# Kernel tuning notes

Measured on AMD Instinct MI355X. Metric: run time of the kernel, lower is better.

The kernel has to match this reference:

```python
import jax, jax.numpy as jnp
import numpy as np

N_NODES = 1_000_000
N_GRAPHS = 8192
DIM = 64
FEAT = 64


def setup_inputs() -> dict:
    key = jax.random.key(0)
    ks = jax.random.split(key, 12)
    s = 0.05
    inp = {}
    inp["x"] = jax.random.normal(ks[0], (N_NODES, FEAT), jnp.float32)
    inp["batch"] = jnp.sort(jax.random.randint(ks[1], (N_NODES,), 0, N_GRAPHS, dtype=jnp.int32))
    inp["lin0_w"] = jax.random.normal(ks[2], (DIM, FEAT), jnp.float32) * s
    inp["lin0_b"] = jnp.zeros((DIM,), jnp.float32)
    inp["lin1_w"] = jax.random.normal(ks[3], (DIM, DIM), jnp.float32) * s
    inp["lin1_b"] = jnp.zeros((DIM,), jnp.float32)
    inp["gru_wih"] = jax.random.normal(ks[4], (3 * DIM, DIM), jnp.float32) * s
    inp["gru_whh"] = jax.random.normal(ks[5], (3 * DIM, DIM), jnp.float32) * s
    inp["gru_bih"] = jnp.zeros((3 * DIM,), jnp.float32)
    inp["gru_bhh"] = jnp.zeros((3 * DIM,), jnp.float32)
    inp["lstm_wih"] = jax.random.normal(ks[6], (4 * DIM, 2 * DIM), jnp.float32) * s
    inp["lstm_whh"] = jax.random.normal(ks[7], (4 * DIM, DIM), jnp.float32) * s
    inp["lstm_bih"] = jnp.zeros((4 * DIM,), jnp.float32)
    inp["lstm_bhh"] = jnp.zeros((4 * DIM,), jnp.float32)
    inp["lin2_w"] = jax.random.normal(ks[8], (DIM, 2 * DIM), jnp.float32) * s
    inp["lin2_b"] = jnp.zeros((DIM,), jnp.float32)
    inp["lin3_w"] = jax.random.normal(ks[9], (1, DIM), jnp.float32) * s
    inp["lin3_b"] = jnp.zeros((1,), jnp.float32)
    inp["n_graphs"] = N_GRAPHS
    return inp


def _gru_step(m, h, wih, whh, bih, bhh):
    # single-step PyTorch GRU semantics
    gi = m @ wih.T + bih          # [N, 3D]
    gh = h @ whh.T + bhh          # [N, 3D]
    ir, iz, in_ = jnp.split(gi, 3, axis=-1)
    hr, hz, hn = jnp.split(gh, 3, axis=-1)
    r = jax.nn.sigmoid(ir + hr)
    z = jax.nn.sigmoid(iz + hz)
    n = jnp.tanh(in_ + r * hn)
    return (1.0 - z) * n + z * h


def _segment_softmax(e, batch, n_graphs):
    m = jax.ops.segment_max(e, batch, num_segments=n_graphs)
    ex = jnp.exp(e - m[batch])
    s = jax.ops.segment_sum(ex, batch, num_segments=n_graphs)
    return ex / (s[batch] + 1e-16)


def reference(x, batch, lin0_w, lin0_b, lin1_w, lin1_b,
              gru_wih, gru_whh, gru_bih, gru_bhh,
              lstm_wih, lstm_whh, lstm_bih, lstm_bhh,
              lin2_w, lin2_b, lin3_w, lin3_b, n_graphs):
    dim = lin0_w.shape[0]
    out = jax.nn.relu(x @ lin0_w.T + lin0_b)   # [N, D]
    h = out
    for _ in range(3):
        m = jax.nn.relu(out @ lin1_w.T + lin1_b)
        h = _gru_step(m, h, gru_wih, gru_whh, gru_bih, gru_bhh)
        out = h

    # Set2Set, processing_steps = 3
    q_star = jnp.zeros((n_graphs, 2 * dim), out.dtype)
    hl = jnp.zeros((n_graphs, dim), out.dtype)
    cl = jnp.zeros((n_graphs, dim), out.dtype)
    for _ in range(3):
        gates = q_star @ lstm_wih.T + lstm_bih + hl @ lstm_whh.T + lstm_bhh  # [B, 4D]
        gi, gf, gg, go = jnp.split(gates, 4, axis=-1)
        cl = jax.nn.sigmoid(gf) * cl + jax.nn.sigmoid(gi) * jnp.tanh(gg)
        hl = jax.nn.sigmoid(go) * jnp.tanh(cl)
        q = hl                                   # [B, D]
        e = jnp.sum(out * q[batch], axis=-1)     # [N]
        a = _segment_softmax(e, batch, n_graphs) # [N]
        r = jax.ops.segment_sum(a[:, None] * out, batch, num_segments=n_graphs)  # [B, D]
        q_star = jnp.concatenate([q, r], axis=-1)

    y = jax.nn.relu(q_star @ lin2_w.T + lin2_b)
    y = y @ lin3_w.T + lin3_b
    return y.reshape(-1)
```

## Files before the change

kernel.cpp:

```cpp
#include <hip/hip_runtime.h>
#include <hip/hip_bf16.h>
#include <math.h>

#define TILES 6
#define MBLK 96

typedef __attribute__((ext_vector_type(8))) short bf8;
typedef __attribute__((ext_vector_type(4))) float f32x4;

#define MFMA(a, b, c) __builtin_amdgcn_mfma_f32_16x16x32_bf16(a, b, c, 0, 0, 0)

__device__ __forceinline__ float fast_rcp(float x) { return __builtin_amdgcn_rcpf(x); }
__device__ __forceinline__ float sigm(float x) { return fast_rcp(1.0f + __expf(-x)); }
__device__ __forceinline__ float tanh2(float x) { return fmaf(2.0f, fast_rcp(1.0f + __expf(-2.0f * x)), -1.0f); }

__device__ __forceinline__ unsigned short f2bf(float v) {
    union { __hip_bfloat16 b; unsigned short u; } cv;
    cv.b = __float2bfloat16(v);
    return cv.u;
}
__device__ __forceinline__ float bf2f(unsigned short u) {
    union { unsigned short u; __hip_bfloat16 b; } cv;
    cv.u = u;
    return __bfloat162float(cv.b);
}
__device__ __forceinline__ void split_tr(float v, unsigned short& hi, unsigned short& lo) {
    unsigned int uv = __builtin_bit_cast(unsigned int, v);
    hi = (unsigned short)(uv >> 16);
    float rem = v - __builtin_bit_cast(float, uv & 0xffff0000u);
    lo = f2bf(rem);
}
__device__ __forceinline__ f32x4 ntload4(const float* p) {
    return __builtin_nontemporal_load((const f32x4*)p);
}

__global__ void prep_kernel(const float* __restrict__ l0w, const float* __restrict__ l1w,
                            const float* __restrict__ gwih, const float* __restrict__ gwhh,
                            const float* __restrict__ lwih, const float* __restrict__ lwhh,
                            const float* __restrict__ l2w,
                            const int* __restrict__ batch,
                            unsigned short* __restrict__ whi, unsigned short* __restrict__ wlo,
                            float* __restrict__ liT, float* __restrict__ lhT,
                            float* __restrict__ l2T,
                            float* __restrict__ u, float* __restrict__ cl,
                            int* __restrict__ startp,
                            int n_nodes, int n_graphs)
{
    int tid = blockIdx.x * 256 + threadIdx.x;
    int nthreads = gridDim.x * 256;
    if (tid < 32768) {
        int e = tid & 7, lane = (tid >> 3) & 63, ks = (tid >> 9) & 1, jt = tid >> 10;
        const float* W; int jl;
        if (jt < 4)       { W = l0w;  jl = jt; }
        else if (jt < 8)  { W = l1w;  jl = jt - 4; }
        else if (jt < 20) { W = gwih; jl = jt - 8; }
        else              { W = gwhh; jl = jt - 20; }
        int j = jl * 16 + (lane & 15);
        int k = ks * 32 + (lane >> 4) * 8 + e;
        float v = W[j * 64 + k];
        unsigned short hi = f2bf(v);
        whi[tid] = hi;
        wlo[tid] = f2bf(v - bf2f(hi));
    }
    if (tid < 32768) liT[tid] = lwih[(tid & 255) * 128 + (tid >> 8)];
    if (tid < 16384) lhT[tid] = lwhh[(tid & 255) * 64 + (tid >> 8)];
    if (tid < 8192)  l2T[tid] = l2w[(tid & 63) * 128 + (tid >> 6)];
    if (tid <= n_graphs) {
        int lo = 0, hi = n_nodes;
        while (lo < hi) {
            int mid = (lo + hi) >> 1;
            if (batch[mid] < tid) lo = mid + 1; else hi = mid;
        }
        startp[tid] = lo;
    }
    for (int i = tid; i < n_graphs * 192; i += nthreads) u[i] = 0.0f;
    for (int i = tid; i < n_graphs * 64;  i += nthreads) cl[i] = 0.0f;
}

__launch_bounds__(256, 2)
__global__ void node_kernel(const float* __restrict__ x,
                            const unsigned short* __restrict__ whi,
                            const unsigned short* __restrict__ wlo,
                            const float* __restrict__ l0b, const float* __restrict__ l1b,
                            const float* __restrict__ gbih, const float* __restrict__ gbhh,
                            float* __restrict__ outv, int n_nodes)
{
    __shared__ unsigned short MHI[TILES * 1024], MLO[TILES * 1024];
    __shared__ unsigned short HHI[TILES * 1024], HLO[TILES * 1024];
    const int tid = threadIdx.x;
    const int w = tid >> 6, lane = tid & 63, c = lane & 15, g = lane >> 4;
    const long node0 = (long)blockIdx.x * MBLK;
    const int j = w * 16 + c;

    const float bR  = gbih[j] + gbhh[j];
    const float bZ  = gbih[64 + j] + gbhh[64 + j];
    const float bNI = gbih[128 + j];
    const float bNH = gbhh[128 + j];
    const float bL1 = l1b[j];
    const float bL0 = l0b[j];

    const int kgj = (j >> 3) & 3;
    const int koff2 = ((j >> 5) * 512) + (kgj * 128) + (j & 7);
    const int lane_swz = (lane & 48) | (c ^ g);

    const bf8* WH = (const bf8*)whi;
    const bf8* WL = (const bf8*)wlo;
#define LF(name, jt) \
    bf8 name##h0 = WH[((jt) * 2 + 0) * 64 + lane], name##h1 = WH[((jt) * 2 + 1) * 64 + lane], \
        name##l0 = WL[((jt) * 2 + 0) * 64 + lane], name##l1 = WL[((jt) * 2 + 1) * 64 + lane];
    LF(w0, w)
    LF(w1, 4 + w)
    LF(gir, 8 + w)  LF(giz, 12 + w)  LF(gin, 16 + w)
    LF(ghr, 20 + w) LF(ghz, 24 + w) LF(ghn, 28 + w)
#undef LF

    float hc[TILES][4];

#pragma unroll
    for (int t = 0; t < TILES; ++t) {
        long nd = node0 + t * 16 + c;
        if (nd >= n_nodes) nd = n_nodes - 1;
        const float* xp = x + nd * 64 + g * 8;
        float va[8], vb[8];
        {
            float4 u0 = *(const float4*)xp;
            float4 u1 = *(const float4*)(xp + 4);
            float4 u2 = *(const float4*)(xp + 32);
            float4 u3 = *(const float4*)(xp + 36);
            va[0] = u0.x; va[1] = u0.y; va[2] = u0.z; va[3] = u0.w;
            va[4] = u1.x; va[5] = u1.y; va[6] = u1.z; va[7] = u1.w;
            vb[0] = u2.x; vb[1] = u2.y; vb[2] = u2.z; vb[3] = u2.w;
            vb[4] = u3.x; vb[5] = u3.y; vb[6] = u3.z; vb[7] = u3.w;
        }
        bf8 xh0, xl0, xh1, xl1;
#pragma unroll
        for (int e = 0; e < 8; ++e) {
            unsigned short h0, l0, h1, l1;
            split_tr(va[e], h0, l0);
            split_tr(vb[e], h1, l1);
            xh0[e] = (short)h0; xl0[e] = (short)l0;
            xh1[e] = (short)h1; xl1[e] = (short)l1;
        }
        f32x4 acc = {bL0, bL0, bL0, bL0};
        acc = MFMA(xh0, w0h0, acc); acc = MFMA(xl0, w0h0, acc); acc = MFMA(xh0, w0l0, acc);
        acc = MFMA(xh1, w0h1, acc); acc = MFMA(xl1, w0h1, acc); acc = MFMA(xh1, w0l1, acc);
#pragma unroll
        for (int p = 0; p < 4; ++p) {
            float hv = fmaxf(acc[p], 0.0f);
            hc[t][p] = hv;
            int r = g * 4 + p;
            unsigned short hi, lo;
            split_tr(hv, hi, lo);
            int idx = t * 1024 + koff2 + ((r ^ kgj) << 3);
            HHI[idx] = hi;
            HLO[idx] = lo;
        }
    }
    __syncthreads();

    for (int iter = 0; iter < 3; ++iter) {
#pragma unroll
        for (int t = 0; t < TILES; ++t) {
            const bf8* hh = (const bf8*)&HHI[t * 1024];
            const bf8* hl = (const bf8*)&HLO[t * 1024];
            bf8 ah0 = hh[lane_swz], ah1 = hh[64 + lane_swz];
            bf8 al0 = hl[lane_swz], al1 = hl[64 + lane_swz];
            f32x4 acc = {bL1, bL1, bL1, bL1};
            acc = MFMA(ah0, w1h0, acc); acc = MFMA(al0, w1h0, acc); acc = MFMA(ah0, w1l0, acc);
            acc = MFMA(ah1, w1h1, acc); acc = MFMA(al1, w1h1, acc); acc = MFMA(ah1, w1l1, acc);
#pragma unroll
            for (int p = 0; p < 4; ++p) {
                float mv = fmaxf(acc[p], 0.0f);
                int r = g * 4 + p;
                unsigned short hi, lo;
                split_tr(mv, hi, lo);
                int idx = t * 1024 + koff2 + ((r ^ kgj) << 3);
                MHI[idx] = hi;
                MLO[idx] = lo;
            }
        }
        __syncthreads();

#pragma unroll
        for (int t = 0; t < TILES; ++t) {
            const bf8* mh = (const bf8*)&MHI[t * 1024];
            const bf8* ml = (const bf8*)&MLO[t * 1024];
            const bf8* hh = (const bf8*)&HHI[t * 1024];
            const bf8* hl = (const bf8*)&HLO[t * 1024];
            bf8 amh0 = mh[lane_swz], amh1 = mh[64 + lane_swz];
            bf8 aml0 = ml[lane_swz], aml1 = ml[64 + lane_swz];
            bf8 ahh0 = hh[lane_swz], ahh1 = hh[64 + lane_swz];
            bf8 ahl0 = hl[lane_swz], ahl1 = hl[64 + lane_swz];

            f32x4 aR  = {bR, bR, bR, bR};
            f32x4 aZ  = {bZ, bZ, bZ, bZ};
            f32x4 aNI = {bNI, bNI, bNI, bNI};
            f32x4 aNH = {bNH, bNH, bNH, bNH};

            aR = MFMA(amh0, girh0, aR); aR = MFMA(aml0, girh0, aR); aR = MFMA(amh0, girl0, aR);
            aR = MFMA(amh1, girh1, aR); aR = MFMA(aml1, girh1, aR); aR = MFMA(amh1, girl1, aR);
            aR = MFMA(ahh0, ghrh0, aR); aR = MFMA(ahl0, ghrh0, aR); aR = MFMA(ahh0, ghrl0, aR);
            aR = MFMA(ahh1, ghrh1, aR); aR = MFMA(ahl1, ghrh1, aR); aR = MFMA(ahh1, ghrl1, aR);

            aZ = MFMA(amh0, gizh0, aZ); aZ = MFMA(aml0, gizh0, aZ); aZ = MFMA(amh0, gizl0, aZ);
            aZ = MFMA(amh1, gizh1, aZ); aZ = MFMA(aml1, gizh1, aZ); aZ = MFMA(amh1, gizl1, aZ);
            aZ = MFMA(ahh0, ghzh0, aZ); aZ = MFMA(ahl0, ghzh0, aZ); aZ = MFMA(ahh0, ghzl0, aZ);
            aZ = MFMA(ahh1, ghzh1, aZ); aZ = MFMA(ahl1, ghzh1, aZ); aZ = MFMA(ahh1, ghzl1, aZ);

            aNI = MFMA(amh0, ginh0, aNI); aNI = MFMA(aml0, ginh0, aNI); aNI = MFMA(amh0, ginl0, aNI);
            aNI = MFMA(amh1, ginh1, aNI); aNI = MFMA(aml1, ginh1, aNI); aNI = MFMA(amh1, ginl1, aNI);

            aNH = MFMA(ahh0, ghnh0, aNH); aNH = MFMA(ahl0, ghnh0, aNH); aNH = MFMA(ahh0, ghnl0, aNH);
            aNH = MFMA(ahh1, ghnh1, aNH); aNH = MFMA(ahl1, ghnh1, aNH); aNH = MFMA(ahh1, ghnl1, aNH);

#pragma unroll
            for (int p = 0; p < 4; ++p) {
                float rg = sigm(aR[p]);
                float zg = sigm(aZ[p]);
                float ng = tanh2(aNI[p] + rg * aNH[p]);
                hc[t][p] = (1.0f - zg) * ng + zg * hc[t][p];
            }
        }

        if (iter < 2) {
            __syncthreads();
#pragma unroll
            for (int t = 0; t < TILES; ++t)
#pragma unroll
                for (int p = 0; p < 4; ++p) {
                    int r = g * 4 + p;
                    unsigned short hi, lo;
                    split_tr(hc[t][p], hi, lo);
                    int idx = t * 1024 + koff2 + ((r ^ kgj) << 3);
                    HHI[idx] = hi;
                    HLO[idx] = lo;
                }
            __syncthreads();
        }
    }

#pragma unroll
    for (int t = 0; t < TILES; ++t)
#pragma unroll
        for (int p = 0; p < 4; ++p) {
            long nd = node0 + t * 16 + g * 4 + p;
            if (nd < n_nodes) outv[nd * 64 + j] = hc[t][p];
        }
}

__global__ void lstm_kernel(const float* __restrict__ liT, const float* __restrict__ lhT,
                            const float* __restrict__ lbih, const float* __restrict__ lbhh,
                            float* __restrict__ u, float* __restrict__ cl, int n_graphs)
{
    const int t = threadIdx.x;
    const int g = blockIdx.x * 4 + (t >> 6);
    const int d = t & 63;
    if (g >= n_graphs) return;
    float* ug = u + (size_t)g * 192;

    float aI = lbih[d]       + lbhh[d];
    float aF = lbih[64 + d]  + lbhh[64 + d];
    float aG = lbih[128 + d] + lbhh[128 + d];
    float aO = lbih[192 + d] + lbhh[192 + d];
    for (int k = 0; k < 128; ++k) {
        float uv = ug[k];
        const float* wr = liT + k * 256;
        aI = fmaf(wr[d], uv, aI);
        aF = fmaf(wr[64 + d], uv, aF);
        aG = fmaf(wr[128 + d], uv, aG);
        aO = fmaf(wr[192 + d], uv, aO);
    }
    for (int k = 0; k < 64; ++k) {
        float hv = ug[128 + k];
        const float* wr = lhT + k * 256;
        aI = fmaf(wr[d], hv, aI);
        aF = fmaf(wr[64 + d], hv, aF);
        aG = fmaf(wr[128 + d], hv, aG);
        aO = fmaf(wr[192 + d], hv, aO);
    }
    float c = sigm(aF) * cl[(size_t)g * 64 + d] + sigm(aI) * tanh2(aG);
    cl[(size_t)g * 64 + d] = c;
    float h = sigm(aO) * tanh2(c);
    ug[d] = h;
    ug[128 + d] = h;
}

__global__ void attn_kernel(const float* __restrict__ outv,
                            const int* __restrict__ startp,
                            float* __restrict__ u, int n_graphs)
{
    __shared__ float qS[64];
    __shared__ float mG[16], sG[16];
    __shared__ float rG[16][64];

    const int g = blockIdx.x;
    const int t = threadIdx.x;
    const int s0 = startp[g];
    const int cnt = startp[g + 1] - s0;
    if (t < 64) qS[t] = u[(size_t)g * 192 + t];
    __syncthreads();

    const int grp = t >> 4, l = t & 15;
    const float q0 = qS[l * 4], q1 = qS[l * 4 + 1], q2 = qS[l * 4 + 2], q3 = qS[l * 4 + 3];

    float m = -INFINITY, s = 0.0f;
    float r0 = 0.0f, r1 = 0.0f, r2 = 0.0f, r3 = 0.0f;

    int n = grp;
    for (; n + 16 < cnt; n += 32) {
        f32x4 va = ntload4(outv + (size_t)(s0 + n) * 64 + l * 4);
        f32x4 vb = ntload4(outv + (size_t)(s0 + n + 16) * 64 + l * 4);
        float ea = fmaf(va.x, q0, fmaf(va.y, q1, fmaf(va.z, q2, va.w * q3)));
        float eb = fmaf(vb.x, q0, fmaf(vb.y, q1, fmaf(vb.z, q2, vb.w * q3)));
#pragma unroll
        for (int o = 1; o < 16; o <<= 1) {
            ea += __shfl_xor(ea, o);
            eb += __shfl_xor(eb, o);
        }
        float mn = fmaxf(m, fmaxf(ea, eb));
        float sc = __expf(m - mn);
        float wa = __expf(ea - mn);
        float wb = __expf(eb - mn);
        s = s * sc + wa + wb;
        r0 = fmaf(r0, sc, fmaf(wa, va.x, wb * vb.x));
        r1 = fmaf(r1, sc, fmaf(wa, va.y, wb * vb.y));
        r2 = fmaf(r2, sc, fmaf(wa, va.z, wb * vb.z));
        r3 = fmaf(r3, sc, fmaf(wa, va.w, wb * vb.w));
        m = mn;
    }
    if (n < cnt) {
        f32x4 va = ntload4(outv + (size_t)(s0 + n) * 64 + l * 4);
        float ea = fmaf(va.x, q0, fmaf(va.y, q1, fmaf(va.z, q2, va.w * q3)));
#pragma unroll
        for (int o = 1; o < 16; o <<= 1) ea += __shfl_xor(ea, o);
        float mn = fmaxf(m, ea);
        float sc = __expf(m - mn);
        float wa = __expf(ea - mn);
        s = s * sc + wa;
        r0 = fmaf(r0, sc, wa * va.x);
        r1 = fmaf(r1, sc, wa * va.y);
        r2 = fmaf(r2, sc, wa * va.z);
        r3 = fmaf(r3, sc, wa * va.w);
        m = mn;
    }

    if (l == 0) { mG[grp] = m; sG[grp] = s; }
    rG[grp][l * 4 + 0] = r0;
    rG[grp][l * 4 + 1] = r1;
    rG[grp][l * 4 + 2] = r2;
    rG[grp][l * 4 + 3] = r3;
    __syncthreads();

    if (t < 64) {
        float M = -INFINITY;
#pragma unroll
        for (int j2 = 0; j2 < 16; ++j2) M = fmaxf(M, mG[j2]);
        float out;
        if (M == -INFINITY) {
            out = 0.0f;
        } else {
            float ssum = 0.0f, racc = 0.0f;
#pragma unroll
            for (int j2 = 0; j2 < 16; ++j2) {
                float sc = __expf(mG[j2] - M);
                ssum = fmaf(sG[j2], sc, ssum);
                racc = fmaf(rG[j2][t], sc, racc);
            }
            out = racc / (ssum + 1e-16f);
        }
        u[(size_t)g * 192 + 64 + t] = out;
    }
}

__global__ void head_kernel(const float* __restrict__ u,
                            const float* __restrict__ l2T, const float* __restrict__ l2b,
                            const float* __restrict__ l3w, const float* __restrict__ l3b,
                            float* __restrict__ yout, int n_graphs)
{
    const int t = threadIdx.x;
    const int g = blockIdx.x * 4 + (t >> 6);
    const int d = t & 63;
    if (g >= n_graphs) return;
    const float* ug = u + (size_t)g * 192;
    float a0 = l2b[d], a1 = 0.0f, a2 = 0.0f, a3 = 0.0f;
    for (int k = 0; k < 128; k += 4) {
        a0 = fmaf(l2T[(k + 0) * 64 + d], ug[k + 0], a0);
        a1 = fmaf(l2T[(k + 1) * 64 + d], ug[k + 1], a1);
        a2 = fmaf(l2T[(k + 2) * 64 + d], ug[k + 2], a2);
        a3 = fmaf(l2T[(k + 3) * 64 + d], ug[k + 3], a3);
    }
    float y = fmaxf((a0 + a1) + (a2 + a3), 0.0f);
    float p = l3w[d] * y;
#pragma unroll
    for (int o = 32; o > 0; o >>= 1) p += __shfl_xor(p, o);
    if (d == 0) yout[g] = p + l3b[0];
}

extern "C" void kernel_launch(void* const* d_in, const int* in_sizes, int n_in,
                              void* d_out, int out_size, void* d_ws, size_t ws_size,
                              hipStream_t stream)
{
    const float* x     = (const float*)d_in[0];
    const int*   batch = (const int*)d_in[1];
    const float* l0w   = (const float*)d_in[2];
    const float* l0b   = (const float*)d_in[3];
    const float* l1w   = (const float*)d_in[4];
    const float* l1b   = (const float*)d_in[5];
    const float* gwih  = (const float*)d_in[6];
    const float* gwhh  = (const float*)d_in[7];
    const float* gbih  = (const float*)d_in[8];
    const float* gbhh  = (const float*)d_in[9];
    const float* lwih  = (const float*)d_in[10];
    const float* lwhh  = (const float*)d_in[11];
    const float* lbih  = (const float*)d_in[12];
    const float* lbhh  = (const float*)d_in[13];
    const float* l2w   = (const float*)d_in[14];
    const float* l2b   = (const float*)d_in[15];
    const float* l3w   = (const float*)d_in[16];
    const float* l3b   = (const float*)d_in[17];

    const int n_nodes  = in_sizes[1];
    const int n_graphs = out_size;

    float* wsf = (float*)d_ws;
    float* outv = wsf;
    float* liT  = wsf + (size_t)n_nodes * 64;
    float* lhT  = liT + 32768;
    float* l2T  = lhT + 16384;
    unsigned short* whi = (unsigned short*)(l2T + 8192);
    unsigned short* wlo = whi + 32768;
    float* u    = (float*)(wlo + 32768);
    float* cl   = u + (size_t)n_graphs * 192;
    int* startp = (int*)(cl + (size_t)n_graphs * 64);

    prep_kernel<<<768, 256, 0, stream>>>(l0w, l1w, gwih, gwhh, lwih, lwhh, l2w, batch,
                                         whi, wlo, liT, lhT, l2T, u, cl, startp,
                                         n_nodes, n_graphs);
    node_kernel<<<(n_nodes + MBLK - 1) / MBLK, 256, 0, stream>>>(
        x, whi, wlo, l0b, l1b, gbih, gbhh, outv, n_nodes);
    for (int step = 0; step < 3; ++step) {
        lstm_kernel<<<(n_graphs + 3) / 4, 256, 0, stream>>>(liT, lhT, lbih, lbhh,
                                                            u, cl, n_graphs);
        attn_kernel<<<n_graphs, 256, 0, stream>>>(outv, startp, u, n_graphs);
    }
    head_kernel<<<(n_graphs + 3) / 4, 256, 0, stream>>>(u, l2T, l2b, l3w, l3b,
                                                        (float*)d_out, n_graphs);
}
```

Baseline: 845.4 us.

## Fuse Set2Set LSTM, attention and head into one kernel; prescale GRU gates

Replaces the seven launches of the Set2Set stage (three LSTM, three attention, one head) with a single kernel. Each block owns four graphs and keeps their LSTM state and q_star in shared memory, so no global u/cl buffers are needed and prep no longer zeroes them. The GRU weights and biases are prescaled by log2(e) so the sigmoid and tanh gates can use exp2 directly, and the gate update is rewritten with FMAs. The node tile grows from 96 to 128 rows, which adds register pressure, and the attention loop now handles one graph at a time inside each block, which lowers parallelism for the attention work.

```diff
diff --git a/kernel.cpp b/kernel.cpp
--- a/kernel.cpp
+++ b/kernel.cpp
@@ -2,8 +2,8 @@
 #include <hip/hip_bf16.h>
 #include <math.h>
 
-#define TILES 6
-#define MBLK 96
+#define TILES 8
+#define MBLK 128
 
 typedef __attribute__((ext_vector_type(8))) short bf8;
 typedef __attribute__((ext_vector_type(4))) float f32x4;
@@ -11,6 +11,15 @@
 #define MFMA(a, b, c) __builtin_amdgcn_mfma_f32_16x16x32_bf16(a, b, c, 0, 0, 0)
 
 __device__ __forceinline__ float fast_rcp(float x) { return __builtin_amdgcn_rcpf(x); }
+#if __has_builtin(__builtin_amdgcn_exp2f)
+__device__ __forceinline__ float exp2b(float x) { return __builtin_amdgcn_exp2f(x); }
+#else
+__device__ __forceinline__ float exp2b(float x) { return exp2f(x); }
+#endif
+__device__ __forceinline__ float sigm2(float xp) { return fast_rcp(1.0f + exp2b(-xp)); }
+__device__ __forceinline__ float tanh2s(float up) {
+    return fmaf(2.0f, fast_rcp(1.0f + exp2b(-up)), -1.0f);
+}
 __device__ __forceinline__ float sigm(float x) { return fast_rcp(1.0f + __expf(-x)); }
 __device__ __forceinline__ float tanh2(float x) { return fmaf(2.0f, fast_rcp(1.0f + __expf(-2.0f * x)), -1.0f); }
 
@@ -42,12 +51,10 @@
                             unsigned short* __restrict__ whi, unsigned short* __restrict__ wlo,
                             float* __restrict__ liT, float* __restrict__ lhT,
                             float* __restrict__ l2T,
-                            float* __restrict__ u, float* __restrict__ cl,
                             int* __restrict__ startp,
                             int n_nodes, int n_graphs)
 {
     int tid = blockIdx.x * 256 + threadIdx.x;
-    int nthreads = gridDim.x * 256;
     if (tid < 32768) {
         int e = tid & 7, lane = (tid >> 3) & 63, ks = (tid >> 9) & 1, jt = tid >> 10;
         const float* W; int jl;
@@ -58,6 +65,7 @@
         int j = jl * 16 + (lane & 15);
         int k = ks * 32 + (lane >> 4) * 8 + e;
         float v = W[j * 64 + k];
+        if (jt >= 8) v *= (j < 128) ? 1.44269504f : 2.88539008f;
         unsigned short hi = f2bf(v);
         whi[tid] = hi;
         wlo[tid] = f2bf(v - bf2f(hi));
@@ -73,8 +81,6 @@
         }
         startp[tid] = lo;
     }
-    for (int i = tid; i < n_graphs * 192; i += nthreads) u[i] = 0.0f;
-    for (int i = tid; i < n_graphs * 64;  i += nthreads) cl[i] = 0.0f;
 }
 
 __launch_bounds__(256, 2)
@@ -92,10 +98,10 @@
     const long node0 = (long)blockIdx.x * MBLK;
     const int j = w * 16 + c;
 
-    const float bR  = gbih[j] + gbhh[j];
-    const float bZ  = gbih[64 + j] + gbhh[64 + j];
-    const float bNI = gbih[128 + j];
-    const float bNH = gbhh[128 + j];
+    const float bR  = (gbih[j] + gbhh[j]) * 1.44269504f;
+    const float bZ  = (gbih[64 + j] + gbhh[64 + j]) * 1.44269504f;
+    const float bNI = gbih[128 + j] * 2.88539008f;
+    const float bNH = gbhh[128 + j] * 2.88539008f;
     const float bL1 = l1b[j];
     const float bL0 = l0b[j];
 
@@ -215,10 +221,10 @@
 
 #pragma unroll
             for (int p = 0; p < 4; ++p) {
-                float rg = sigm(aR[p]);
-                float zg = sigm(aZ[p]);
-                float ng = tanh2(aNI[p] + rg * aNH[p]);
-                hc[t][p] = (1.0f - zg) * ng + zg * hc[t][p];
+                float rg = sigm2(aR[p]);
+                float zg = sigm2(aZ[p]);
+                float ng = tanh2s(fmaf(rg, aNH[p], aNI[p]));
+                hc[t][p] = fmaf(zg, hc[t][p] - ng, ng);
             }
         }
 
@@ -248,152 +254,153 @@
         }
 }
 
-__global__ void lstm_kernel(const float* __restrict__ liT, const float* __restrict__ lhT,
-                            const float* __restrict__ lbih, const float* __restrict__ lbhh,
-                            float* __restrict__ u, float* __restrict__ cl, int n_graphs)
+__global__ void s2s_kernel(const float* __restrict__ outv,
+                           const int* __restrict__ startp,
+                           const float* __restrict__ liT, const float* __restrict__ lhT,
+                           const float* __restrict__ lbih, const float* __restrict__ lbhh,
+                           const float* __restrict__ l2T, const float* __restrict__ l2b,
+                           const float* __restrict__ l3w, const float* __restrict__ l3b,
+                           float* __restrict__ yout, int n_graphs)
 {
-    const int t = threadIdx.x;
-    const int g = blockIdx.x * 4 + (t >> 6);
-    const int d = t & 63;
-    if (g >= n_graphs) return;
-    float* ug = u + (size_t)g * 192;
-
-    float aI = lbih[d]       + lbhh[d];
-    float aF = lbih[64 + d]  + lbhh[64 + d];
-    float aG = lbih[128 + d] + lbhh[128 + d];
-    float aO = lbih[192 + d] + lbhh[192 + d];
-    for (int k = 0; k < 128; ++k) {
-        float uv = ug[k];
-        const float* wr = liT + k * 256;
-        aI = fmaf(wr[d], uv, aI);
-        aF = fmaf(wr[64 + d], uv, aF);
-        aG = fmaf(wr[128 + d], uv, aG);
-        aO = fmaf(wr[192 + d], uv, aO);
-    }
-    for (int k = 0; k < 64; ++k) {
-        float hv = ug[128 + k];
-        const float* wr = lhT + k * 256;
-        aI = fmaf(wr[d], hv, aI);
-        aF = fmaf(wr[64 + d], hv, aF);
-        aG = fmaf(wr[128 + d], hv, aG);
-        aO = fmaf(wr[192 + d], hv, aO);
-    }
-    float c = sigm(aF) * cl[(size_t)g * 64 + d] + sigm(aI) * tanh2(aG);
-    cl[(size_t)g * 64 + d] = c;
-    float h = sigm(aO) * tanh2(c);
-    ug[d] = h;
-    ug[128 + d] = h;
-}
-
-__global__ void attn_kernel(const float* __restrict__ outv,
-                            const int* __restrict__ startp,
-                            float* __restrict__ u, int n_graphs)
-{
-    __shared__ float qS[64];
+    __shared__ float uS[4][192];
+    __shared__ float clS[4][64];
     __shared__ float mG[16], sG[16];
     __shared__ float rG[16][64];
 
-    const int g = blockIdx.x;
     const int t = threadIdx.x;
-    const int s0 = startp[g];
-    const int cnt = startp[g + 1] - s0;
-    if (t < 64) qS[t] = u[(size_t)g * 192 + t];
+    const int w = t >> 6, lane = t & 63;
+    const int gbase = blockIdx.x * 4;
+    const int grp = t >> 4, l = t & 15;
+
+    uS[w][lane] = 0.0f; uS[w][64 + lane] = 0.0f; uS[w][128 + lane] = 0.0f;
+    clS[w][lane] = 0.0f;
     __syncthreads();
 
-    const int grp = t >> 4, l = t & 15;
-    const float q0 = qS[l * 4], q1 = qS[l * 4 + 1], q2 = qS[l * 4 + 2], q3 = qS[l * 4 + 3];
-
-    float m = -INFINITY, s = 0.0f;
-    float r0 = 0.0f, r1 = 0.0f, r2 = 0.0f, r3 = 0.0f;
-
-    int n = grp;
-    for (; n + 16 < cnt; n += 32) {
-        f32x4 va = ntload4(outv + (size_t)(s0 + n) * 64 + l * 4);
-        f32x4 vb = ntload4(outv + (size_t)(s0 + n + 16) * 64 + l * 4);
-        float ea = fmaf(va.x, q0, fmaf(va.y, q1, fmaf(va.z, q2, va.w * q3)));
-        float eb = fmaf(vb.x, q0, fmaf(vb.y, q1, fmaf(vb.z, q2, vb.w * q3)));
-#pragma unroll
-        for (int o = 1; o < 16; o <<= 1) {
-            ea += __shfl_xor(ea, o);
-            eb += __shfl_xor(eb, o);
-        }
-        float mn = fmaxf(m, fmaxf(ea, eb));
-        float sc = __expf(m - mn);
-        float wa = __expf(ea - mn);
-        float wb = __expf(eb - mn);
-        s = s * sc + wa + wb;
-        r0 = fmaf(r0, sc, fmaf(wa, va.x, wb * vb.x));
-        r1 = fmaf(r1, sc, fmaf(wa, va.y, wb * vb.y));
-        r2 = fmaf(r2, sc, fmaf(wa, va.z, wb * vb.z));
-        r3 = fmaf(r3, sc, fmaf(wa, va.w, wb * vb.w));
-        m = mn;
-    }
-    if (n < cnt) {
-        f32x4 va = ntload4(outv + (size_t)(s0 + n) * 64 + l * 4);
-        float ea = fmaf(va.x, q0, fmaf(va.y, q1, fmaf(va.z, q2, va.w * q3)));
-#pragma unroll
-        for (int o = 1; o < 16; o <<= 1) ea += __shfl_xor(ea, o);
-        float mn = fmaxf(m, ea);
-        float sc = __expf(m - mn);
-        float wa = __expf(ea - mn);
-        s = s * sc + wa;
-        r0 = fmaf(r0, sc, wa * va.x);
-        r1 = fmaf(r1, sc, wa * va.y);
-        r2 = fmaf(r2, sc, wa * va.z);
-        r3 = fmaf(r3, sc, wa * va.w);
-        m = mn;
-    }
-
-    if (l == 0) { mG[grp] = m; sG[grp] = s; }
-    rG[grp][l * 4 + 0] = r0;
-    rG[grp][l * 4 + 1] = r1;
-    rG[grp][l * 4 + 2] = r2;
-    rG[grp][l * 4 + 3] = r3;
-    __syncthreads();
-
-    if (t < 64) {
-        float M = -INFINITY;
-#pragma unroll
-        for (int j2 = 0; j2 < 16; ++j2) M = fmaxf(M, mG[j2]);
-        float out;
-        if (M == -INFINITY) {
-            out = 0.0f;
-        } else {
-            float ssum = 0.0f, racc = 0.0f;
-#pragma unroll
-            for (int j2 = 0; j2 < 16; ++j2) {
-                float sc = __expf(mG[j2] - M);
-                ssum = fmaf(sG[j2], sc, ssum);
-                racc = fmaf(rG[j2][t], sc, racc);
-            }
-            out = racc / (ssum + 1e-16f);
-        }
-        u[(size_t)g * 192 + 64 + t] = out;
-    }
-}
-
-__global__ void head_kernel(const float* __restrict__ u,
-                            const float* __restrict__ l2T, const float* __restrict__ l2b,
-                            const float* __restrict__ l3w, const float* __restrict__ l3b,
-                            float* __restrict__ yout, int n_graphs)
-{
-    const int t = threadIdx.x;
-    const int g = blockIdx.x * 4 + (t >> 6);
-    const int d = t & 63;
-    if (g >= n_graphs) return;
-    const float* ug = u + (size_t)g * 192;
-    float a0 = l2b[d], a1 = 0.0f, a2 = 0.0f, a3 = 0.0f;
-    for (int k = 0; k < 128; k += 4) {
-        a0 = fmaf(l2T[(k + 0) * 64 + d], ug[k + 0], a0);
-        a1 = fmaf(l2T[(k + 1) * 64 + d], ug[k + 1], a1);
-        a2 = fmaf(l2T[(k + 2) * 64 + d], ug[k + 2], a2);
-        a3 = fmaf(l2T[(k + 3) * 64 + d], ug[k + 3], a3);
-    }
-    float y = fmaxf((a0 + a1) + (a2 + a3), 0.0f);
-    float p = l3w[d] * y;
-#pragma unroll
-    for (int o = 32; o > 0; o >>= 1) p += __shfl_xor(p, o);
-    if (d == 0) yout[g] = p + l3b[0];
+    for (int step = 0; step < 3; ++step) {
+        {
+            const int d = lane;
+            float aI = lbih[d]       + lbhh[d];
+            float aF = lbih[64 + d]  + lbhh[64 + d];
+            float aG = lbih[128 + d] + lbhh[128 + d];
+            float aO = lbih[192 + d] + lbhh[192 + d];
+            for (int k = 0; k < 128; ++k) {
+                float uv = uS[w][k];
+                const float* wr = liT + k * 256;
+                aI = fmaf(wr[d], uv, aI);
+                aF = fmaf(wr[64 + d], uv, aF);
+                aG = fmaf(wr[128 + d], uv, aG);
+                aO = fmaf(wr[192 + d], uv, aO);
+            }
+            for (int k = 0; k < 64; ++k) {
+                float hv = uS[w][128 + k];
+                const float* wr = lhT + k * 256;
+                aI = fmaf(wr[d], hv, aI);
+                aF = fmaf(wr[64 + d], hv, aF);
+                aG = fmaf(wr[128 + d], hv, aG);
+                aO = fmaf(wr[192 + d], hv, aO);
+            }
+            float c = sigm(aF) * clS[w][d] + sigm(aI) * tanh2(aG);
+            clS[w][d] = c;
+            float h = sigm(aO) * tanh2(c);
+            uS[w][d] = h;
+            uS[w][128 + d] = h;
+        }
+        __syncthreads();
+
+        for (int idx = 0; idx < 4; ++idx) {
+            const int g = gbase + idx;
+            int s0 = 0, cnt = 0;
+            if (g < n_graphs) { s0 = startp[g]; cnt = startp[g + 1] - s0; }
+
+            const float q0 = uS[idx][l * 4 + 0], q1 = uS[idx][l * 4 + 1];
+            const float q2 = uS[idx][l * 4 + 2], q3 = uS[idx][l * 4 + 3];
+
+            float m = -INFINITY, s = 0.0f;
+            float r0 = 0.0f, r1 = 0.0f, r2 = 0.0f, r3 = 0.0f;
+
+            int n = grp;
+            for (; n + 16 < cnt; n += 32) {
+                f32x4 va = ntload4(outv + (size_t)(s0 + n) * 64 + l * 4);
+                f32x4 vb = ntload4(outv + (size_t)(s0 + n + 16) * 64 + l * 4);
+                float ea = fmaf(va.x, q0, fmaf(va.y, q1, fmaf(va.z, q2, va.w * q3)));
+                float eb = fmaf(vb.x, q0, fmaf(vb.y, q1, fmaf(vb.z, q2, vb.w * q3)));
+#pragma unroll
+                for (int o = 1; o < 16; o <<= 1) {
+                    ea += __shfl_xor(ea, o);
+                    eb += __shfl_xor(eb, o);
+                }
+                float mn = fmaxf(m, fmaxf(ea, eb));
+                float sc = __expf(m - mn);
+                float wa = __expf(ea - mn);
+                float wb = __expf(eb - mn);
+                s = s * sc + wa + wb;
+                r0 = fmaf(r0, sc, fmaf(wa, va.x, wb * vb.x));
+                r1 = fmaf(r1, sc, fmaf(wa, va.y, wb * vb.y));
+                r2 = fmaf(r2, sc, fmaf(wa, va.z, wb * vb.z));
+                r3 = fmaf(r3, sc, fmaf(wa, va.w, wb * vb.w));
+                m = mn;
+            }
+            if (n < cnt) {
+                f32x4 va = ntload4(outv + (size_t)(s0 + n) * 64 + l * 4);
+                float ea = fmaf(va.x, q0, fmaf(va.y, q1, fmaf(va.z, q2, va.w * q3)));
+#pragma unroll
+                for (int o = 1; o < 16; o <<= 1) ea += __shfl_xor(ea, o);
+                float mn = fmaxf(m, ea);
+                float sc = __expf(m - mn);
+                float wa = __expf(ea - mn);
+                s = s * sc + wa;
+                r0 = fmaf(r0, sc, wa * va.x);
+                r1 = fmaf(r1, sc, wa * va.y);
+                r2 = fmaf(r2, sc, wa * va.z);
+                r3 = fmaf(r3, sc, wa * va.w);
+                m = mn;
+            }
+
+            if (l == 0) { mG[grp] = m; sG[grp] = s; }
+            rG[grp][l * 4 + 0] = r0;
+            rG[grp][l * 4 + 1] = r1;
+            rG[grp][l * 4 + 2] = r2;
+            rG[grp][l * 4 + 3] = r3;
+            __syncthreads();
+
+            if (t < 64) {
+                float M = -INFINITY;
+#pragma unroll
+                for (int j2 = 0; j2 < 16; ++j2) M = fmaxf(M, mG[j2]);
+                float out;
+                if (M == -INFINITY) {
+                    out = 0.0f;
+                } else {
+                    float ssum = 0.0f, racc = 0.0f;
+#pragma unroll
+                    for (int j2 = 0; j2 < 16; ++j2) {
+                        float sc = __expf(mG[j2] - M);
+                        ssum = fmaf(sG[j2], sc, ssum);
+                        racc = fmaf(rG[j2][t], sc, racc);
+                    }
+                    out = racc / (ssum + 1e-16f);
+                }
+                uS[idx][64 + t] = out;
+            }
+            __syncthreads();
+        }
+    }
+
+    {
+        const int d = lane;
+        float a0 = l2b[d], a1 = 0.0f, a2 = 0.0f, a3 = 0.0f;
+        for (int k = 0; k < 128; k += 4) {
+            a0 = fmaf(l2T[(k + 0) * 64 + d], uS[w][k + 0], a0);
+            a1 = fmaf(l2T[(k + 1) * 64 + d], uS[w][k + 1], a1);
+            a2 = fmaf(l2T[(k + 2) * 64 + d], uS[w][k + 2], a2);
+            a3 = fmaf(l2T[(k + 3) * 64 + d], uS[w][k + 3], a3);
+        }
+        float y = fmaxf((a0 + a1) + (a2 + a3), 0.0f);
+        float p = l3w[d] * y;
+#pragma unroll
+        for (int o = 32; o > 0; o >>= 1) p += __shfl_xor(p, o);
+        if (d == 0 && gbase + w < n_graphs) yout[gbase + w] = p + l3b[0];
+    }
 }
 
 extern "C" void kernel_launch(void* const* d_in, const int* in_sizes, int n_in,
@@ -429,20 +436,14 @@
     float* l2T  = lhT + 16384;
     unsigned short* whi = (unsigned short*)(l2T + 8192);
     unsigned short* wlo = whi + 32768;
-    float* u    = (float*)(wlo + 32768);
-    float* cl   = u + (size_t)n_graphs * 192;
-    int* startp = (int*)(cl + (size_t)n_graphs * 64);
-
-    prep_kernel<<<768, 256, 0, stream>>>(l0w, l1w, gwih, gwhh, lwih, lwhh, l2w, batch,
-                                         whi, wlo, liT, lhT, l2T, u, cl, startp,
+    int* startp = (int*)(wlo + 32768);
+
+    prep_kernel<<<128, 256, 0, stream>>>(l0w, l1w, gwih, gwhh, lwih, lwhh, l2w, batch,
+                                         whi, wlo, liT, lhT, l2T, startp,
                                          n_nodes, n_graphs);
     node_kernel<<<(n_nodes + MBLK - 1) / MBLK, 256, 0, stream>>>(
         x, whi, wlo, l0b, l1b, gbih, gbhh, outv, n_nodes);
-    for (int step = 0; step < 3; ++step) {
-        lstm_kernel<<<(n_graphs + 3) / 4, 256, 0, stream>>>(liT, lhT, lbih, lbhh,
-                                                            u, cl, n_graphs);
-        attn_kernel<<<n_graphs, 256, 0, stream>>>(outv, startp, u, n_graphs);
-    }
-    head_kernel<<<(n_graphs + 3) / 4, 256, 0, stream>>>(u, l2T, l2b, l3w, l3b,
-                                                        (float*)d_out, n_graphs);
-}
+    s2s_kernel<<<(n_graphs + 3) / 4, 256, 0, stream>>>(
+        outv, startp, liT, lhT, lbih, lbhh, l2T, l2b, l3w, l3b,
+        (float*)d_out, n_graphs);
+}
```

New measurement: 768.5 us. -9.1%, faster.
